# Kernel tuning notes

Measured on AMD Instinct MI355X. Metric: run time of the kernel, lower is better.

The kernel has to match this reference:

```python
import jax, jax.numpy as jnp
import numpy as np

EPS = 1e-6
LN_EPS = 1e-5


def setup_inputs() -> dict:
    key = jax.random.key(0)
    k1, k2, k3 = jax.random.split(key, 3)
    N, L, H, D = 4, 16384, 8, 16
    return {
        "queries": jax.random.normal(k1, (N, L, H, D), dtype=jnp.float32),
        "keys": jax.random.normal(k2, (N, L, H, D), dtype=jnp.float32),
        "values": jax.random.normal(k3, (N, L, H, D), dtype=jnp.float32),
        "ln_gamma": jnp.ones((D,), dtype=jnp.float32),
        "ln_beta": jnp.zeros((D,), dtype=jnp.float32),
    }


def reference(queries, keys, values, ln_gamma, ln_beta):
    initial = values  # [N, L, H, D]
    # to [N, H, L, D] and apply sigmoid feature map
    q = jax.nn.sigmoid(jnp.transpose(queries, (0, 2, 1, 3)))
    k = jax.nn.sigmoid(jnp.transpose(keys, (0, 2, 1, 3)))
    v = jnp.transpose(values, (0, 2, 1, 3))
    L = q.shape[2]
    S = k.shape[2]
    # competition/allocation normalizers (flow attention)
    normalizer_row = 1.0 / jnp.einsum('nhld,nhd->nhl', q + EPS, k.sum(axis=2) + EPS)
    normalizer_col = 1.0 / jnp.einsum('nhsd,nhd->nhs', k + EPS, q.sum(axis=2) + EPS)
    normalizer_row_refine = jnp.einsum(
        'nhld,nhd->nhl', q + EPS, (k * normalizer_col[..., None]).sum(axis=2) + EPS)
    normalizer_col_refine = jnp.einsum(
        'nhsd,nhd->nhs', k + EPS, (q * normalizer_row[..., None]).sum(axis=2) + EPS)
    normalizer_row_refine = jax.nn.sigmoid(normalizer_row_refine * (float(L) / float(S)))
    normalizer_col_refine = jax.nn.softmax(normalizer_col_refine, axis=-1) * S
    # linear attention: K^T @ (V * col_refine), then Q @ kv
    kv = jnp.einsum('nhsd,nhse->nhde', k, v * normalizer_col_refine[..., None])  # [N,H,D,D]
    x = jnp.einsum('nhld,nhde->nhle', q, kv)
    x = x * normalizer_row[..., None] * normalizer_row_refine[..., None]
    x = jnp.transpose(x, (0, 2, 1, 3))  # [N, L, H, D]
    x = initial + x
    # LayerNorm over last dim (D=16), biased variance as in torch
    mean = jnp.mean(x, axis=-1, keepdims=True)
    var = jnp.mean(jnp.square(x - mean), axis=-1, keepdims=True)
    x = (x - mean) / jnp.sqrt(var + LN_EPS) * ln_gamma + ln_beta
    return x
```

## Files before the change

### kernel.cpp

```cpp
#include <hip/hip_runtime.h>
#include <math.h>
#include <stdint.h>

constexpr int LL = 16384;
constexpr int NROW = 65536;
constexpr int NPAIR = NROW * 8;
constexpr int PAIRS_PER_N = NPAIR / 4;
constexpr float EPS = 1e-6f;
constexpr float LN_EPS = 1e-5f;

constexpr int OFF_QSUM = 0;
constexpr int OFF_KSUM = 512;
constexpr int OFF_QN   = 1024;
constexpr int OFF_KN   = 1536;
constexpr int OFF_SSUM = 2048;
constexpr int OFF_KVU  = 2080;
constexpr int STATS_FLOATS = OFF_KVU + 4 * 2048;
constexpr int FLOAT_END = 10304;
constexpr size_t MIR_Q_BYTE = (size_t)FLOAT_END * 4;
constexpr size_t MIR_ELEMS  = (size_t)NPAIR * 16;
constexpr size_t MIR_K_BYTE = MIR_Q_BYTE + MIR_ELEMS * 2;
constexpr size_t WS_FULL    = MIR_K_BYTE + MIR_ELEMS * 2;

__device__ __forceinline__ float sigm(float x) { return __fdividef(1.f, 1.f + __expf(-x)); }
__device__ __forceinline__ unsigned short f2bf(float f) {
  uint32_t x = __float_as_uint(f);
  return (unsigned short)((x + 0x7FFFu + ((x >> 16) & 1u)) >> 16);
}
__device__ __forceinline__ float bf2f(unsigned short u) {
  return __uint_as_float(((uint32_t)u) << 16);
}

template <bool MIR>
__device__ __forceinline__ void load_sig(const unsigned short* mir, const float* fp, int p, float* r) {
  if (MIR) {
    const uint4* p4 = reinterpret_cast<const uint4*>(mir + (size_t)p * 16);
    uint4 a = p4[0], b = p4[1];
    uint32_t w[8] = {a.x, a.y, a.z, a.w, b.x, b.y, b.z, b.w};
#pragma unroll
    for (int j = 0; j < 8; ++j) {
      r[2 * j]     = bf2f((unsigned short)(w[j] & 0xFFFFu));
      r[2 * j + 1] = bf2f((unsigned short)(w[j] >> 16));
    }
  } else {
    const float4* p4 = reinterpret_cast<const float4*>(fp + (size_t)p * 16);
#pragma unroll
    for (int j = 0; j < 4; ++j) {
      float4 a = p4[j];
      r[4 * j] = sigm(a.x); r[4 * j + 1] = sigm(a.y);
      r[4 * j + 2] = sigm(a.z); r[4 * j + 3] = sigm(a.w);
    }
  }
}
__device__ __forceinline__ void load_raw16(const float* fp, int p, float* r) {
  const float4* p4 = reinterpret_cast<const float4*>(fp + (size_t)p * 16);
#pragma unroll
  for (int j = 0; j < 4; ++j) {
    float4 a = p4[j];
    r[4 * j] = a.x; r[4 * j + 1] = a.y; r[4 * j + 2] = a.z; r[4 * j + 3] = a.w;
  }
}

__device__ __forceinline__ float hred(float v) {
  v += __shfl_xor(v, 8, 64);
  v += __shfl_xor(v, 16, 64);
  v += __shfl_xor(v, 32, 64);
  return v;
}

__device__ __forceinline__ void stat_atomic2(float* q, float* k, float* dQ, float* dK, int tid) {
  __shared__ float w4[4][256];
  const int wave = tid >> 6, lane = tid & 63;
#pragma unroll
  for (int d = 0; d < 16; ++d) { q[d] = hred(q[d]); k[d] = hred(k[d]); }
  if (lane < 8) {
#pragma unroll
    for (int d = 0; d < 16; ++d) {
      w4[wave][lane * 16 + d] = q[d];
      w4[wave][128 + lane * 16 + d] = k[d];
    }
  }
  __syncthreads();
  const float v = w4[0][tid] + w4[1][tid] + w4[2][tid] + w4[3][tid];
  if (tid < 128) atomicAdd(dQ + tid, v);
  else atomicAdd(dK + (tid - 128), v);
}

__device__ __forceinline__ void stat_atomic1(float* q, float* dQ, int tid) {
  __shared__ float w1[4][128];
  const int wave = tid >> 6, lane = tid & 63;
#pragma unroll
  for (int d = 0; d < 16; ++d) q[d] = hred(q[d]);
  if (lane < 8) {
#pragma unroll
    for (int d = 0; d < 16; ++d) w1[wave][lane * 16 + d] = q[d];
  }
  __syncthreads();
  if (tid < 128) atomicAdd(dQ + tid, w1[0][tid] + w1[1][tid] + w1[2][tid] + w1[3][tid]);
}

__global__ __launch_bounds__(256) void k_zero(float4* ws4) {
  const int i = blockIdx.x * 256 + threadIdx.x;
  if (i < STATS_FLOATS / 4) ws4[i] = make_float4(0.f, 0.f, 0.f, 0.f);
}

template <bool MIR>
__global__ __launch_bounds__(256) void k_prep(const float* __restrict__ Q, const float* __restrict__ K,
                                              float* __restrict__ ws,
                                              unsigned short* __restrict__ sQ, unsigned short* __restrict__ sK) {
  const int tid = threadIdx.x;
  const int n = blockIdx.x >> 7;
  const int b = blockIdx.x & 127;
  float sq[16], sk[16];
#pragma unroll
  for (int d = 0; d < 16; ++d) { sq[d] = 0.f; sk[d] = 0.f; }
#pragma unroll
  for (int c = 0; c < 4; ++c) {
    const int p = n * PAIRS_PER_N + (b * 4 + c) * 256 + tid;
    float q[16], k[16];
    load_sig<false>(nullptr, Q, p, q);
    load_sig<false>(nullptr, K, p, k);
    if (MIR) {
      union U { unsigned short u[8]; uint4 v; };
      U a, bb;
#pragma unroll
      for (int j = 0; j < 8; ++j) { a.u[j] = f2bf(q[j]); bb.u[j] = f2bf(q[8 + j]); }
      uint4* dq = reinterpret_cast<uint4*>(sQ + (size_t)p * 16);
      dq[0] = a.v; dq[1] = bb.v;
#pragma unroll
      for (int j = 0; j < 8; ++j) { a.u[j] = f2bf(k[j]); bb.u[j] = f2bf(k[8 + j]); }
      uint4* dk = reinterpret_cast<uint4*>(sK + (size_t)p * 16);
      dk[0] = a.v; dk[1] = bb.v;
    }
#pragma unroll
    for (int d = 0; d < 16; ++d) { sq[d] += q[d]; sk[d] += k[d]; }
  }
  stat_atomic2(sq, sk, ws + OFF_QSUM + n * 128, ws + OFF_KSUM + n * 128, tid);
}

template <bool MIR>
__global__ __launch_bounds__(256) void k_refq(const float* __restrict__ Q,
                                              const unsigned short* __restrict__ sQ,
                                              float* __restrict__ ws) {
  const int tid = threadIdx.x;
  const int n = blockIdx.x >> 7;
  const int b = blockIdx.x & 127;
  __shared__ float ksE[128];
  if (tid < 128) ksE[tid] = ws[OFF_KSUM + n * 128 + tid] + EPS;
  __syncthreads();
  const int h = tid & 7;
  float qn[16];
#pragma unroll
  for (int d = 0; d < 16; ++d) qn[d] = 0.f;
#pragma unroll
  for (int c = 0; c < 4; ++c) {
    const int p = n * PAIRS_PER_N + (b * 4 + c) * 256 + tid;
    float q[16];
    load_sig<MIR>(sQ, Q, p, q);
    float dr = 0.f;
#pragma unroll
    for (int d = 0; d < 16; ++d) dr += (q[d] + EPS) * ksE[h * 16 + d];
    const float nr = __fdividef(1.f, dr);
#pragma unroll
    for (int d = 0; d < 16; ++d) qn[d] += q[d] * nr;
  }
  stat_atomic1(qn, ws + OFF_QN + n * 128, tid);
}

template <bool MIR>
__global__ __launch_bounds__(256) void k_kv(const float* __restrict__ K, const float* __restrict__ V,
                                            const unsigned short* __restrict__ sK,
                                            float* __restrict__ ws) {
  const int tid = threadIdx.x;
  const int n = blockIdx.x >> 6;
  const int b = blockIdx.x & 63;
  constexpr int RS = 132;
  __shared__ float qnE[128], qsE[128];
  __shared__ float ssb[8];
  __shared__ __align__(16) float kwL[32 * RS];
  __shared__ __align__(16) float vL[32 * RS];
  if (tid < 128) {
    qnE[tid] = ws[OFF_QN + n * 128 + tid] + EPS;
    qsE[tid] = ws[OFF_QSUM + n * 128 + tid] + EPS;
  }
  if (tid < 8) ssb[tid] = 0.f;
  __syncthreads();
  const int h = tid & 7, ri = tid >> 3, lane = tid & 63;
  const int h2 = tid >> 5;
  const int d0 = ((tid >> 2) & 7) * 2;
  const int e0 = (tid & 3) * 4;
  const int base = n * PAIRS_PER_N + b * 2048;
  float acc[2][4] = {{0.f, 0.f, 0.f, 0.f}, {0.f, 0.f, 0.f, 0.f}};
  float kn[16];
#pragma unroll
  for (int d = 0; d < 16; ++d) kn[d] = 0.f;
  float kb[2][16], vb[2][16];
  load_sig<MIR>(sK, K, base + tid, kb[0]);
  load_raw16(V, base + tid, vb[0]);
#pragma unroll 2
  for (int t = 0; t < 8; ++t) {
    const int cur = t & 1, nxt = cur ^ 1;
    float* k = kb[cur];
    float* v = vb[cur];
    float dc = 0.f, ncr = 0.f;
#pragma unroll
    for (int d = 0; d < 16; ++d) {
      const float ke = k[d] + EPS;
      dc += ke * qsE[h * 16 + d];
      ncr += ke * qnE[h * 16 + d];
    }
    const float nc = __fdividef(1.f, dc);
#pragma unroll
    for (int d = 0; d < 16; ++d) kn[d] += k[d] * nc;
    const float w = __expf(ncr);
    float sw = hred(w);
    if (lane < 8) atomicAdd(&ssb[lane], sw);
    const int wb = ri * RS + h * 16;
#pragma unroll
    for (int d = 0; d < 16; ++d) { kwL[wb + d] = k[d] * w; vL[wb + d] = v[d]; }
    if (t < 7) {
      load_sig<MIR>(sK, K, base + (t + 1) * 256 + tid, kb[nxt]);
      load_raw16(V, base + (t + 1) * 256 + tid, vb[nxt]);
    }
    __syncthreads();
    const int rb0 = h2 * 16;
#pragma unroll 4
    for (int r = 0; r < 32; ++r) {
      const int rb = r * RS + rb0;
      const float2 kk = *reinterpret_cast<const float2*>(&kwL[rb + d0]);
      const float4 vv = *reinterpret_cast<const float4*>(&vL[rb + e0]);
      acc[0][0] += kk.x * vv.x; acc[0][1] += kk.x * vv.y;
      acc[0][2] += kk.x * vv.z; acc[0][3] += kk.x * vv.w;
      acc[1][0] += kk.y * vv.x; acc[1][1] += kk.y * vv.y;
      acc[1][2] += kk.y * vv.z; acc[1][3] += kk.y * vv.w;
    }
    __syncthreads();
  }
  stat_atomic1(kn, ws + OFF_KN + n * 128, tid);
  if (tid < 8) atomicAdd(&ws[OFF_SSUM + n * 8 + tid], ssb[tid]);
  float* kv = ws + OFF_KVU + n * 2048 + h2 * 256;
#pragma unroll
  for (int j = 0; j < 4; ++j) atomicAdd(&kv[d0 * 16 + e0 + j], acc[0][j]);
#pragma unroll
  for (int j = 0; j < 4; ++j) atomicAdd(&kv[(d0 + 1) * 16 + e0 + j], acc[1][j]);
}

template <bool MIR>
__global__ __launch_bounds__(256) void k_out(const float* __restrict__ Q, const float* __restrict__ V,
                                             const unsigned short* __restrict__ sQ,
                                             const float* __restrict__ gamma, const float* __restrict__ beta,
                                             const float* __restrict__ ws, float* __restrict__ out) {
  const int tid = threadIdx.x;
  const int p = blockIdx.x * 256 + tid;
  const int n = blockIdx.x >> 9;
  __shared__ __align__(16) float kvs[8 * 260];
  __shared__ float ksE[128], knE[128], gm[16], bt[16], ssE[8];
  if (tid < 8) ssE[tid] = __fdividef((float)LL, ws[OFF_SSUM + n * 8 + tid]);
  if (tid >= 8 && tid < 136) {
    const int i = tid - 8;
    ksE[i] = ws[OFF_KSUM + n * 128 + i] + EPS;
    knE[i] = ws[OFF_KN + n * 128 + i] + EPS;
  }
  if (tid >= 136 && tid < 152) gm[tid - 136] = gamma[tid - 136];
  else if (tid >= 152 && tid < 168) bt[tid - 152] = beta[tid - 152];
  __syncthreads();
  for (int i = tid; i < 2048; i += 256) {
    const int hh = i >> 8, de = i & 255;
    kvs[hh * 260 + de] = ws[OFF_KVU + n * 2048 + i] * ssE[hh];
  }
  __syncthreads();
  const int h = tid & 7;
  float q[16], v[16];
  load_sig<MIR>(sQ, Q, p, q);
  load_raw16(V, p, v);
  float dr = 0.f, drr = 0.f;
#pragma unroll
  for (int d = 0; d < 16; ++d) {
    const float qe = q[d] + EPS;
    dr += qe * ksE[h * 16 + d];
    drr += qe * knE[h * 16 + d];
  }
  const float sc = __fdividef(1.f, dr) * sigm(drr);
  float x[16];
#pragma unroll
  for (int e = 0; e < 16; ++e) x[e] = 0.f;
#pragma unroll
  for (int d = 0; d < 16; ++d) {
    const float qd = q[d];
    const float4* kr = reinterpret_cast<const float4*>(&kvs[h * 260 + d * 16]);
#pragma unroll
    for (int j = 0; j < 4; ++j) {
      float4 a = kr[j];
      x[4 * j] += qd * a.x; x[4 * j + 1] += qd * a.y;
      x[4 * j + 2] += qd * a.z; x[4 * j + 3] += qd * a.w;
    }
  }
#pragma unroll
  for (int e = 0; e < 16; ++e) x[e] = x[e] * sc + v[e];
  float mean = 0.f;
#pragma unroll
  for (int e = 0; e < 16; ++e) mean += x[e];
  mean *= (1.f / 16.f);
  float var = 0.f;
#pragma unroll
  for (int e = 0; e < 16; ++e) { const float t = x[e] - mean; var += t * t; }
  var *= (1.f / 16.f);
  const float inv = rsqrtf(var + LN_EPS);
#pragma unroll
  for (int e = 0; e < 16; ++e) x[e] = (x[e] - mean) * inv * gm[e] + bt[e];
  float4* op = reinterpret_cast<float4*>(out + (size_t)p * 16);
  op[0] = make_float4(x[0], x[1], x[2], x[3]);
  op[1] = make_float4(x[4], x[5], x[6], x[7]);
  op[2] = make_float4(x[8], x[9], x[10], x[11]);
  op[3] = make_float4(x[12], x[13], x[14], x[15]);
}

extern "C" void kernel_launch(void* const* d_in, const int* in_sizes, int n_in,
                              void* d_out, int out_size, void* d_ws, size_t ws_size,
                              hipStream_t stream) {
  const float* Q = (const float*)d_in[0];
  const float* K = (const float*)d_in[1];
  const float* V = (const float*)d_in[2];
  const float* gamma = (const float*)d_in[3];
  const float* beta = (const float*)d_in[4];
  float* ws = (float*)d_ws;
  float* out = (float*)d_out;
  unsigned short* sQ = (unsigned short*)((char*)d_ws + MIR_Q_BYTE);
  unsigned short* sK = (unsigned short*)((char*)d_ws + MIR_K_BYTE);

  const dim3 blk(256);
  const int gPrep = 512;
  const int gKv = 256;
  const int gOut = NPAIR / 256;
  const int gZero = (STATS_FLOATS / 4 + 255) / 256;

  k_zero<<<gZero, blk, 0, stream>>>(reinterpret_cast<float4*>(ws));
  if (ws_size >= WS_FULL) {
    k_prep<true><<<gPrep, blk, 0, stream>>>(Q, K, ws, sQ, sK);
    k_refq<true><<<gPrep, blk, 0, stream>>>(Q, sQ, ws);
    k_kv<true><<<gKv, blk, 0, stream>>>(K, V, sK, ws);
    k_out<true><<<gOut, blk, 0, stream>>>(Q, V, sQ, gamma, beta, ws, out);
  } else {
    k_prep<false><<<gPrep, blk, 0, stream>>>(Q, K, ws, nullptr, nullptr);
    k_refq<false><<<gPrep, blk, 0, stream>>>(Q, nullptr, ws);
    k_kv<false><<<gKv, blk, 0, stream>>>(K, V, nullptr, ws);
    k_out<false><<<gOut, blk, 0, stream>>>(Q, V, nullptr, gamma, beta, ws, out);
  }
}
```

Measured before the change: 190.8 us.

## Replicate atomic accumulators across eight slots and double k_kv grid

Global statistic accumulators (qsum, ksum, qn, kn, softmax sums, kv) are split into eight replicas indexed by block, so fewer blocks contend on the same atomic addresses. Consumer kernels sum the replicas when loading. Separately, k_kv now launches twice as many blocks, each handling half the rows, for more parallelism. The cost is extra reads of the replicas in every consumer block, a larger zeroing pass, and more atomics issued overall by k_kv.

```diff
diff --git a/kernel.cpp b/kernel.cpp
--- a/kernel.cpp
+++ b/kernel.cpp
@@ -8,15 +8,16 @@
 constexpr int PAIRS_PER_N = NPAIR / 4;
 constexpr float EPS = 1e-6f;
 constexpr float LN_EPS = 1e-5f;
+constexpr int NREP = 8;
 
 constexpr int OFF_QSUM = 0;
-constexpr int OFF_KSUM = 512;
-constexpr int OFF_QN   = 1024;
-constexpr int OFF_KN   = 1536;
-constexpr int OFF_SSUM = 2048;
-constexpr int OFF_KVU  = 2080;
-constexpr int STATS_FLOATS = OFF_KVU + 4 * 2048;
-constexpr int FLOAT_END = 10304;
+constexpr int OFF_KSUM = OFF_QSUM + 4096;
+constexpr int OFF_QN   = OFF_KSUM + 4096;
+constexpr int OFF_KN   = OFF_QN + 4096;
+constexpr int OFF_SSUM = OFF_KN + 4096;
+constexpr int OFF_KVU  = OFF_SSUM + 256;
+constexpr int STATS_FLOATS = OFF_KVU + 4 * NREP * 2048;
+constexpr int FLOAT_END = STATS_FLOATS;
 constexpr size_t MIR_Q_BYTE = (size_t)FLOAT_END * 4;
 constexpr size_t MIR_ELEMS  = (size_t)NPAIR * 16;
 constexpr size_t MIR_K_BYTE = MIR_Q_BYTE + MIR_ELEMS * 2;
@@ -97,6 +98,13 @@
   }
   __syncthreads();
   if (tid < 128) atomicAdd(dQ + tid, w1[0][tid] + w1[1][tid] + w1[2][tid] + w1[3][tid]);
+}
+
+__device__ __forceinline__ float rep_sum128(const float* base, int n, int i) {
+  float v = 0.f;
+#pragma unroll
+  for (int r = 0; r < NREP; ++r) v += base[(n * NREP + r) * 128 + i];
+  return v;
 }
 
 __global__ __launch_bounds__(256) void k_zero(float4* ws4) {
@@ -111,6 +119,7 @@
   const int tid = threadIdx.x;
   const int n = blockIdx.x >> 7;
   const int b = blockIdx.x & 127;
+  const int rep = b & (NREP - 1);
   float sq[16], sk[16];
 #pragma unroll
   for (int d = 0; d < 16; ++d) { sq[d] = 0.f; sk[d] = 0.f; }
@@ -135,7 +144,8 @@
 #pragma unroll
     for (int d = 0; d < 16; ++d) { sq[d] += q[d]; sk[d] += k[d]; }
   }
-  stat_atomic2(sq, sk, ws + OFF_QSUM + n * 128, ws + OFF_KSUM + n * 128, tid);
+  stat_atomic2(sq, sk, ws + OFF_QSUM + (n * NREP + rep) * 128,
+               ws + OFF_KSUM + (n * NREP + rep) * 128, tid);
 }
 
 template <bool MIR>
@@ -145,8 +155,9 @@
   const int tid = threadIdx.x;
   const int n = blockIdx.x >> 7;
   const int b = blockIdx.x & 127;
+  const int rep = b & (NREP - 1);
   __shared__ float ksE[128];
-  if (tid < 128) ksE[tid] = ws[OFF_KSUM + n * 128 + tid] + EPS;
+  if (tid < 128) ksE[tid] = rep_sum128(ws + OFF_KSUM, n, tid) + EPS;
   __syncthreads();
   const int h = tid & 7;
   float qn[16];
@@ -164,7 +175,7 @@
 #pragma unroll
     for (int d = 0; d < 16; ++d) qn[d] += q[d] * nr;
   }
-  stat_atomic1(qn, ws + OFF_QN + n * 128, tid);
+  stat_atomic1(qn, ws + OFF_QN + (n * NREP + rep) * 128, tid);
 }
 
 template <bool MIR>
@@ -172,16 +183,17 @@
                                             const unsigned short* __restrict__ sK,
                                             float* __restrict__ ws) {
   const int tid = threadIdx.x;
-  const int n = blockIdx.x >> 6;
-  const int b = blockIdx.x & 63;
+  const int n = blockIdx.x >> 7;
+  const int b = blockIdx.x & 127;
+  const int rep = b & (NREP - 1);
   constexpr int RS = 132;
   __shared__ float qnE[128], qsE[128];
   __shared__ float ssb[8];
   __shared__ __align__(16) float kwL[32 * RS];
   __shared__ __align__(16) float vL[32 * RS];
   if (tid < 128) {
-    qnE[tid] = ws[OFF_QN + n * 128 + tid] + EPS;
-    qsE[tid] = ws[OFF_QSUM + n * 128 + tid] + EPS;
+    qnE[tid] = rep_sum128(ws + OFF_QN, n, tid) + EPS;
+    qsE[tid] = rep_sum128(ws + OFF_QSUM, n, tid) + EPS;
   }
   if (tid < 8) ssb[tid] = 0.f;
   __syncthreads();
@@ -189,7 +201,7 @@
   const int h2 = tid >> 5;
   const int d0 = ((tid >> 2) & 7) * 2;
   const int e0 = (tid & 3) * 4;
-  const int base = n * PAIRS_PER_N + b * 2048;
+  const int base = n * PAIRS_PER_N + b * 1024;
   float acc[2][4] = {{0.f, 0.f, 0.f, 0.f}, {0.f, 0.f, 0.f, 0.f}};
   float kn[16];
 #pragma unroll
@@ -198,7 +210,7 @@
   load_sig<MIR>(sK, K, base + tid, kb[0]);
   load_raw16(V, base + tid, vb[0]);
 #pragma unroll 2
-  for (int t = 0; t < 8; ++t) {
+  for (int t = 0; t < 4; ++t) {
     const int cur = t & 1, nxt = cur ^ 1;
     float* k = kb[cur];
     float* v = vb[cur];
@@ -218,7 +230,7 @@
     const int wb = ri * RS + h * 16;
 #pragma unroll
     for (int d = 0; d < 16; ++d) { kwL[wb + d] = k[d] * w; vL[wb + d] = v[d]; }
-    if (t < 7) {
+    if (t < 3) {
       load_sig<MIR>(sK, K, base + (t + 1) * 256 + tid, kb[nxt]);
       load_raw16(V, base + (t + 1) * 256 + tid, vb[nxt]);
     }
@@ -236,9 +248,9 @@
     }
     __syncthreads();
   }
-  stat_atomic1(kn, ws + OFF_KN + n * 128, tid);
-  if (tid < 8) atomicAdd(&ws[OFF_SSUM + n * 8 + tid], ssb[tid]);
-  float* kv = ws + OFF_KVU + n * 2048 + h2 * 256;
+  stat_atomic1(kn, ws + OFF_KN + (n * NREP + rep) * 128, tid);
+  if (tid < 8) atomicAdd(&ws[OFF_SSUM + (n * NREP + rep) * 8 + tid], ssb[tid]);
+  float* kv = ws + OFF_KVU + (size_t)(n * NREP + rep) * 2048 + h2 * 256;
 #pragma unroll
   for (int j = 0; j < 4; ++j) atomicAdd(&kv[d0 * 16 + e0 + j], acc[0][j]);
 #pragma unroll
@@ -255,18 +267,26 @@
   const int n = blockIdx.x >> 9;
   __shared__ __align__(16) float kvs[8 * 260];
   __shared__ float ksE[128], knE[128], gm[16], bt[16], ssE[8];
-  if (tid < 8) ssE[tid] = __fdividef((float)LL, ws[OFF_SSUM + n * 8 + tid]);
+  if (tid < 8) {
+    float ss = 0.f;
+#pragma unroll
+    for (int r = 0; r < NREP; ++r) ss += ws[OFF_SSUM + (n * NREP + r) * 8 + tid];
+    ssE[tid] = __fdividef((float)LL, ss);
+  }
   if (tid >= 8 && tid < 136) {
     const int i = tid - 8;
-    ksE[i] = ws[OFF_KSUM + n * 128 + i] + EPS;
-    knE[i] = ws[OFF_KN + n * 128 + i] + EPS;
+    ksE[i] = rep_sum128(ws + OFF_KSUM, n, i) + EPS;
+    knE[i] = rep_sum128(ws + OFF_KN, n, i) + EPS;
   }
   if (tid >= 136 && tid < 152) gm[tid - 136] = gamma[tid - 136];
   else if (tid >= 152 && tid < 168) bt[tid - 152] = beta[tid - 152];
   __syncthreads();
   for (int i = tid; i < 2048; i += 256) {
     const int hh = i >> 8, de = i & 255;
-    kvs[hh * 260 + de] = ws[OFF_KVU + n * 2048 + i] * ssE[hh];
+    float acc = 0.f;
+#pragma unroll
+    for (int r = 0; r < NREP; ++r) acc += ws[OFF_KVU + (size_t)(n * NREP + r) * 2048 + i];
+    kvs[hh * 260 + de] = acc * ssE[hh];
   }
   __syncthreads();
   const int h = tid & 7;
@@ -330,7 +350,7 @@
 
   const dim3 blk(256);
   const int gPrep = 512;
-  const int gKv = 256;
+  const int gKv = 512;
   const int gOut = NPAIR / 256;
   const int gZero = (STATS_FLOATS / 4 + 255) / 256;
 
```

After: 202.4 us. 1.06x slower.

## Replace global atomics with per-block partials and add a reduction kernel

Applied to the files above, without the earlier changes.

Each stats kernel now writes per-block partial sums to workspace instead of atomically adding into shared totals. Consumers reduce those partials on load, and a new k_kvred kernel folds the kv, kn, softmax-sum and ksum partials. This removes the zeroing kernel and the atomic contention. It also lets k_kv run with four times as many blocks, each handling 512 pairs, for better occupancy. In exchange the workspace grows, there is one extra launch, and every block of k_refq and k_kv redundantly re-reduces the partials.

```diff
diff --git a/kernel.cpp b/kernel.cpp
--- a/kernel.cpp
+++ b/kernel.cpp
@@ -9,14 +9,16 @@
 constexpr float EPS = 1e-6f;
 constexpr float LN_EPS = 1e-5f;
 
-constexpr int OFF_QSUM = 0;
-constexpr int OFF_KSUM = 512;
-constexpr int OFF_QN   = 1024;
-constexpr int OFF_KN   = 1536;
-constexpr int OFF_SSUM = 2048;
-constexpr int OFF_KVU  = 2080;
-constexpr int STATS_FLOATS = OFF_KVU + 4 * 2048;
-constexpr int FLOAT_END = 10304;
+constexpr int F_KSUM = 0;
+constexpr int F_KN   = 512;
+constexpr int F_SS   = 1024;
+constexpr int F_KV   = 1056;
+constexpr int P_A1 = 9472;
+constexpr int P_A2 = P_A1 + 4 * 128 * 256;
+constexpr int P_KN = P_A2 + 4 * 128 * 128;
+constexpr int P_SS = P_KN + 4 * 256 * 128;
+constexpr int P_KV = P_SS + 4 * 256 * 8;
+constexpr int FLOAT_END = P_KV + 4 * 256 * 2048;
 constexpr size_t MIR_Q_BYTE = (size_t)FLOAT_END * 4;
 constexpr size_t MIR_ELEMS  = (size_t)NPAIR * 16;
 constexpr size_t MIR_K_BYTE = MIR_Q_BYTE + MIR_ELEMS * 2;
@@ -68,40 +70,33 @@
   return v;
 }
 
-__device__ __forceinline__ void stat_atomic2(float* q, float* k, float* dQ, float* dK, int tid) {
-  __shared__ float w4[4][256];
+__device__ __forceinline__ void stat_partial2(float* a, float* b, float* w4 ,
+                                              float* dst, int tid) {
   const int wave = tid >> 6, lane = tid & 63;
 #pragma unroll
-  for (int d = 0; d < 16; ++d) { q[d] = hred(q[d]); k[d] = hred(k[d]); }
+  for (int d = 0; d < 16; ++d) { a[d] = hred(a[d]); b[d] = hred(b[d]); }
   if (lane < 8) {
 #pragma unroll
     for (int d = 0; d < 16; ++d) {
-      w4[wave][lane * 16 + d] = q[d];
-      w4[wave][128 + lane * 16 + d] = k[d];
+      w4[wave * 256 + lane * 16 + d] = a[d];
+      w4[wave * 256 + 128 + lane * 16 + d] = b[d];
     }
   }
   __syncthreads();
-  const float v = w4[0][tid] + w4[1][tid] + w4[2][tid] + w4[3][tid];
-  if (tid < 128) atomicAdd(dQ + tid, v);
-  else atomicAdd(dK + (tid - 128), v);
-}
-
-__device__ __forceinline__ void stat_atomic1(float* q, float* dQ, int tid) {
-  __shared__ float w1[4][128];
+  dst[tid] = w4[tid] + w4[256 + tid] + w4[512 + tid] + w4[768 + tid];
+}
+
+__device__ __forceinline__ void stat_partial1(float* a, float* w1 ,
+                                              float* dst, int tid) {
   const int wave = tid >> 6, lane = tid & 63;
 #pragma unroll
-  for (int d = 0; d < 16; ++d) q[d] = hred(q[d]);
+  for (int d = 0; d < 16; ++d) a[d] = hred(a[d]);
   if (lane < 8) {
 #pragma unroll
-    for (int d = 0; d < 16; ++d) w1[wave][lane * 16 + d] = q[d];
+    for (int d = 0; d < 16; ++d) w1[wave * 128 + lane * 16 + d] = a[d];
   }
   __syncthreads();
-  if (tid < 128) atomicAdd(dQ + tid, w1[0][tid] + w1[1][tid] + w1[2][tid] + w1[3][tid]);
-}
-
-__global__ __launch_bounds__(256) void k_zero(float4* ws4) {
-  const int i = blockIdx.x * 256 + threadIdx.x;
-  if (i < STATS_FLOATS / 4) ws4[i] = make_float4(0.f, 0.f, 0.f, 0.f);
+  if (tid < 128) dst[tid] = w1[tid] + w1[128 + tid] + w1[256 + tid] + w1[384 + tid];
 }
 
 template <bool MIR>
@@ -111,6 +106,7 @@
   const int tid = threadIdx.x;
   const int n = blockIdx.x >> 7;
   const int b = blockIdx.x & 127;
+  __shared__ float w4[1024];
   float sq[16], sk[16];
 #pragma unroll
   for (int d = 0; d < 16; ++d) { sq[d] = 0.f; sk[d] = 0.f; }
@@ -135,7 +131,7 @@
 #pragma unroll
     for (int d = 0; d < 16; ++d) { sq[d] += q[d]; sk[d] += k[d]; }
   }
-  stat_atomic2(sq, sk, ws + OFF_QSUM + n * 128, ws + OFF_KSUM + n * 128, tid);
+  stat_partial2(sq, sk, w4, ws + P_A1 + (size_t)blockIdx.x * 256, tid);
 }
 
 template <bool MIR>
@@ -146,8 +142,18 @@
   const int n = blockIdx.x >> 7;
   const int b = blockIdx.x & 127;
   __shared__ float ksE[128];
-  if (tid < 128) ksE[tid] = ws[OFF_KSUM + n * 128 + tid] + EPS;
-  __syncthreads();
+  __shared__ float w1[512];
+  {
+    const int i = tid & 127, half = tid >> 7;
+    float a = 0.f;
+    const float* src = ws + P_A1 + ((size_t)(n * 128 + half * 64)) * 256 + 128 + i;
+#pragma unroll 4
+    for (int c = 0; c < 64; ++c) a += src[(size_t)c * 256];
+    w1[tid] = a;
+    __syncthreads();
+    if (tid < 128) ksE[tid] = w1[tid] + w1[128 + tid] + EPS;
+    __syncthreads();
+  }
   const int h = tid & 7;
   float qn[16];
 #pragma unroll
@@ -164,7 +170,7 @@
 #pragma unroll
     for (int d = 0; d < 16; ++d) qn[d] += q[d] * nr;
   }
-  stat_atomic1(qn, ws + OFF_QN + n * 128, tid);
+  stat_partial1(qn, w1, ws + P_A2 + (size_t)blockIdx.x * 128, tid);
 }
 
 template <bool MIR>
@@ -172,24 +178,39 @@
                                             const unsigned short* __restrict__ sK,
                                             float* __restrict__ ws) {
   const int tid = threadIdx.x;
-  const int n = blockIdx.x >> 6;
-  const int b = blockIdx.x & 63;
+  const int n = blockIdx.x >> 8;
+  const int b = blockIdx.x & 255;
   constexpr int RS = 132;
   __shared__ float qnE[128], qsE[128];
   __shared__ float ssb[8];
+  __shared__ float w1[512];
   __shared__ __align__(16) float kwL[32 * RS];
   __shared__ __align__(16) float vL[32 * RS];
-  if (tid < 128) {
-    qnE[tid] = ws[OFF_QN + n * 128 + tid] + EPS;
-    qsE[tid] = ws[OFF_QSUM + n * 128 + tid] + EPS;
-  }
-  if (tid < 8) ssb[tid] = 0.f;
-  __syncthreads();
+  {
+    const int i = tid & 127, half = tid >> 7;
+    float a = 0.f;
+    const float* src = ws + P_A1 + ((size_t)(n * 128 + half * 64)) * 256 + i;
+#pragma unroll 4
+    for (int c = 0; c < 64; ++c) a += src[(size_t)c * 256];
+    w1[tid] = a;
+    __syncthreads();
+    if (tid < 128) qsE[tid] = w1[tid] + w1[128 + tid] + EPS;
+    __syncthreads();
+    float bb = 0.f;
+    const float* src2 = ws + P_A2 + ((size_t)(n * 128 + half * 64)) * 128 + i;
+#pragma unroll 4
+    for (int c = 0; c < 64; ++c) bb += src2[(size_t)c * 128];
+    w1[tid] = bb;
+    __syncthreads();
+    if (tid < 128) qnE[tid] = w1[tid] + w1[128 + tid] + EPS;
+    if (tid < 8) ssb[tid] = 0.f;
+    __syncthreads();
+  }
   const int h = tid & 7, ri = tid >> 3, lane = tid & 63;
   const int h2 = tid >> 5;
   const int d0 = ((tid >> 2) & 7) * 2;
   const int e0 = (tid & 3) * 4;
-  const int base = n * PAIRS_PER_N + b * 2048;
+  const int base = n * PAIRS_PER_N + b * 512;
   float acc[2][4] = {{0.f, 0.f, 0.f, 0.f}, {0.f, 0.f, 0.f, 0.f}};
   float kn[16];
 #pragma unroll
@@ -197,11 +218,10 @@
   float kb[2][16], vb[2][16];
   load_sig<MIR>(sK, K, base + tid, kb[0]);
   load_raw16(V, base + tid, vb[0]);
-#pragma unroll 2
-  for (int t = 0; t < 8; ++t) {
-    const int cur = t & 1, nxt = cur ^ 1;
-    float* k = kb[cur];
-    float* v = vb[cur];
+#pragma unroll
+  for (int t = 0; t < 2; ++t) {
+    float* k = kb[t];
+    float* v = vb[t];
     float dc = 0.f, ncr = 0.f;
 #pragma unroll
     for (int d = 0; d < 16; ++d) {
@@ -218,9 +238,9 @@
     const int wb = ri * RS + h * 16;
 #pragma unroll
     for (int d = 0; d < 16; ++d) { kwL[wb + d] = k[d] * w; vL[wb + d] = v[d]; }
-    if (t < 7) {
-      load_sig<MIR>(sK, K, base + (t + 1) * 256 + tid, kb[nxt]);
-      load_raw16(V, base + (t + 1) * 256 + tid, vb[nxt]);
+    if (t < 1) {
+      load_sig<MIR>(sK, K, base + 256 + tid, kb[1]);
+      load_raw16(V, base + 256 + tid, vb[1]);
     }
     __syncthreads();
     const int rb0 = h2 * 16;
@@ -236,13 +256,46 @@
     }
     __syncthreads();
   }
-  stat_atomic1(kn, ws + OFF_KN + n * 128, tid);
-  if (tid < 8) atomicAdd(&ws[OFF_SSUM + n * 8 + tid], ssb[tid]);
-  float* kv = ws + OFF_KVU + n * 2048 + h2 * 256;
-#pragma unroll
-  for (int j = 0; j < 4; ++j) atomicAdd(&kv[d0 * 16 + e0 + j], acc[0][j]);
-#pragma unroll
-  for (int j = 0; j < 4; ++j) atomicAdd(&kv[(d0 + 1) * 16 + e0 + j], acc[1][j]);
+  stat_partial1(kn, w1, ws + P_KN + (size_t)blockIdx.x * 128, tid);
+  if (tid < 8) ws[P_SS + (size_t)blockIdx.x * 8 + tid] = ssb[tid];
+  float* pk = ws + P_KV + (size_t)blockIdx.x * 2048;
+  *reinterpret_cast<float4*>(pk + h2 * 256 + d0 * 16 + e0) =
+      make_float4(acc[0][0], acc[0][1], acc[0][2], acc[0][3]);
+  *reinterpret_cast<float4*>(pk + h2 * 256 + (d0 + 1) * 16 + e0) =
+      make_float4(acc[1][0], acc[1][1], acc[1][2], acc[1][3]);
+}
+
+__global__ __launch_bounds__(256) void k_kvred(float* __restrict__ ws) {
+  const int tid = threadIdx.x;
+  const int n = blockIdx.x >> 3, seg = blockIdx.x & 7;
+  {
+    float a = 0.f;
+    const float* src = ws + P_KV + (size_t)n * 256 * 2048 + seg * 256 + tid;
+#pragma unroll 4
+    for (int c = 0; c < 256; ++c) a += src[(size_t)c * 2048];
+    ws[F_KV + n * 2048 + seg * 256 + tid] = a;
+  }
+  if (seg == 0 && tid < 128) {
+    float s = 0.f;
+    const float* src = ws + P_KN + (size_t)n * 256 * 128 + tid;
+#pragma unroll 4
+    for (int c = 0; c < 256; ++c) s += src[(size_t)c * 128];
+    ws[F_KN + n * 128 + tid] = s;
+  }
+  if (seg == 1 && tid < 8) {
+    float s = 0.f;
+    const float* src = ws + P_SS + (size_t)n * 256 * 8 + tid;
+#pragma unroll 4
+    for (int c = 0; c < 256; ++c) s += src[(size_t)c * 8];
+    ws[F_SS + n * 8 + tid] = s;
+  }
+  if (seg == 2 && tid < 128) {
+    float s = 0.f;
+    const float* src = ws + P_A1 + (size_t)n * 128 * 256 + 128 + tid;
+#pragma unroll 4
+    for (int c = 0; c < 128; ++c) s += src[(size_t)c * 256];
+    ws[F_KSUM + n * 128 + tid] = s;
+  }
 }
 
 template <bool MIR>
@@ -255,18 +308,18 @@
   const int n = blockIdx.x >> 9;
   __shared__ __align__(16) float kvs[8 * 260];
   __shared__ float ksE[128], knE[128], gm[16], bt[16], ssE[8];
-  if (tid < 8) ssE[tid] = __fdividef((float)LL, ws[OFF_SSUM + n * 8 + tid]);
+  if (tid < 8) ssE[tid] = __fdividef((float)LL, ws[F_SS + n * 8 + tid]);
   if (tid >= 8 && tid < 136) {
     const int i = tid - 8;
-    ksE[i] = ws[OFF_KSUM + n * 128 + i] + EPS;
-    knE[i] = ws[OFF_KN + n * 128 + i] + EPS;
+    ksE[i] = ws[F_KSUM + n * 128 + i] + EPS;
+    knE[i] = ws[F_KN + n * 128 + i] + EPS;
   }
   if (tid >= 136 && tid < 152) gm[tid - 136] = gamma[tid - 136];
   else if (tid >= 152 && tid < 168) bt[tid - 152] = beta[tid - 152];
   __syncthreads();
   for (int i = tid; i < 2048; i += 256) {
     const int hh = i >> 8, de = i & 255;
-    kvs[hh * 260 + de] = ws[OFF_KVU + n * 2048 + i] * ssE[hh];
+    kvs[hh * 260 + de] = ws[F_KV + n * 2048 + i] * ssE[hh];
   }
   __syncthreads();
   const int h = tid & 7;
@@ -330,20 +383,20 @@
 
   const dim3 blk(256);
   const int gPrep = 512;
-  const int gKv = 256;
+  const int gKv = 1024;
   const int gOut = NPAIR / 256;
-  const int gZero = (STATS_FLOATS / 4 + 255) / 256;
-
-  k_zero<<<gZero, blk, 0, stream>>>(reinterpret_cast<float4*>(ws));
+
   if (ws_size >= WS_FULL) {
     k_prep<true><<<gPrep, blk, 0, stream>>>(Q, K, ws, sQ, sK);
     k_refq<true><<<gPrep, blk, 0, stream>>>(Q, sQ, ws);
     k_kv<true><<<gKv, blk, 0, stream>>>(K, V, sK, ws);
+    k_kvred<<<32, blk, 0, stream>>>(ws);
     k_out<true><<<gOut, blk, 0, stream>>>(Q, V, sQ, gamma, beta, ws, out);
   } else {
     k_prep<false><<<gPrep, blk, 0, stream>>>(Q, K, ws, nullptr, nullptr);
     k_refq<false><<<gPrep, blk, 0, stream>>>(Q, nullptr, ws);
     k_kv<false><<<gKv, blk, 0, stream>>>(K, V, nullptr, ws);
+    k_kvred<<<32, blk, 0, stream>>>(ws);
     k_out<false><<<gOut, blk, 0, stream>>>(Q, V, nullptr, gamma, beta, ws, out);
   }
 }
```

New measurement: 234.8 us. +23.1%, slower.

## Replace float atomics with per-block partials and last-block reductions

Applied to the files above, without the earlier changes.

Each stats kernel now writes per-block partial sums to workspace slots. A counter-based last-block pattern lets the final block of each batch reduce those partials and write the totals, replacing float atomicAdd accumulation. This also removes the separate zeroing kernel launch. The counters are never reset, so correctness relies on the modulo-TARGET wraparound and on the workspace starting at zero. The final reduction now runs serially in a single block per batch.

```diff
diff --git a/kernel.cpp b/kernel.cpp
--- a/kernel.cpp
+++ b/kernel.cpp
@@ -8,17 +8,24 @@
 constexpr int PAIRS_PER_N = NPAIR / 4;
 constexpr float EPS = 1e-6f;
 constexpr float LN_EPS = 1e-5f;
-
-constexpr int OFF_QSUM = 0;
-constexpr int OFF_KSUM = 512;
-constexpr int OFF_QN   = 1024;
-constexpr int OFF_KN   = 1536;
-constexpr int OFF_SSUM = 2048;
-constexpr int OFF_KVU  = 2080;
-constexpr int STATS_FLOATS = OFF_KVU + 4 * 2048;
-constexpr int FLOAT_END = 10304;
+constexpr size_t MIR_ELEMS = (size_t)NPAIR * 16;
+
+constexpr int F_KSUM = 0;
+constexpr int F_KN   = 512;
+constexpr int F_SS   = 1024;
+constexpr int F_QSUM = 1056;
+constexpr int F_QN   = 1568;
+constexpr int F_KV   = 2080;
+constexpr int CNT_A  = 10272;
+constexpr int CNT_B  = 10276;
+constexpr int CNT_C  = 10280;
+constexpr int P_A1 = 10304;
+constexpr int P_A2 = P_A1 + 512 * 256;
+constexpr int P_KN = P_A2 + 512 * 128;
+constexpr int P_SS = P_KN + 256 * 128;
+constexpr int P_KV = P_SS + 256 * 8;
+constexpr int FLOAT_END = P_KV + 256 * 2048;
 constexpr size_t MIR_Q_BYTE = (size_t)FLOAT_END * 4;
-constexpr size_t MIR_ELEMS  = (size_t)NPAIR * 16;
 constexpr size_t MIR_K_BYTE = MIR_Q_BYTE + MIR_ELEMS * 2;
 constexpr size_t WS_FULL    = MIR_K_BYTE + MIR_ELEMS * 2;
 
@@ -60,6 +67,14 @@
     r[4 * j] = a.x; r[4 * j + 1] = a.y; r[4 * j + 2] = a.z; r[4 * j + 3] = a.w;
   }
 }
+__device__ __forceinline__ void pack_store(unsigned short* dst, int p, const float* r) {
+  union U { unsigned short u[8]; uint4 v; };
+  U a, b;
+#pragma unroll
+  for (int j = 0; j < 8; ++j) { a.u[j] = f2bf(r[j]); b.u[j] = f2bf(r[8 + j]); }
+  uint4* d = reinterpret_cast<uint4*>(dst + (size_t)p * 16);
+  d[0] = a.v; d[1] = b.v;
+}
 
 __device__ __forceinline__ float hred(float v) {
   v += __shfl_xor(v, 8, 64);
@@ -68,40 +83,47 @@
   return v;
 }
 
-__device__ __forceinline__ void stat_atomic2(float* q, float* k, float* dQ, float* dK, int tid) {
-  __shared__ float w4[4][256];
+__device__ __forceinline__ void stat_partial2(float* a, float* b, float* w4 ,
+                                              float* dst, int tid) {
   const int wave = tid >> 6, lane = tid & 63;
 #pragma unroll
-  for (int d = 0; d < 16; ++d) { q[d] = hred(q[d]); k[d] = hred(k[d]); }
+  for (int d = 0; d < 16; ++d) { a[d] = hred(a[d]); b[d] = hred(b[d]); }
   if (lane < 8) {
 #pragma unroll
     for (int d = 0; d < 16; ++d) {
-      w4[wave][lane * 16 + d] = q[d];
-      w4[wave][128 + lane * 16 + d] = k[d];
-    }
-  }
-  __syncthreads();
-  const float v = w4[0][tid] + w4[1][tid] + w4[2][tid] + w4[3][tid];
-  if (tid < 128) atomicAdd(dQ + tid, v);
-  else atomicAdd(dK + (tid - 128), v);
-}
-
-__device__ __forceinline__ void stat_atomic1(float* q, float* dQ, int tid) {
-  __shared__ float w1[4][128];
+      w4[wave * 256 + lane * 16 + d] = a[d];
+      w4[wave * 256 + 128 + lane * 16 + d] = b[d];
+    }
+  }
+  __syncthreads();
+  dst[tid] = w4[tid] + w4[256 + tid] + w4[512 + tid] + w4[768 + tid];
+}
+
+__device__ __forceinline__ void stat_partial1(float* a, float* w1 ,
+                                              float* dst, int tid) {
   const int wave = tid >> 6, lane = tid & 63;
 #pragma unroll
-  for (int d = 0; d < 16; ++d) q[d] = hred(q[d]);
+  for (int d = 0; d < 16; ++d) a[d] = hred(a[d]);
   if (lane < 8) {
 #pragma unroll
-    for (int d = 0; d < 16; ++d) w1[wave][lane * 16 + d] = q[d];
-  }
-  __syncthreads();
-  if (tid < 128) atomicAdd(dQ + tid, w1[0][tid] + w1[1][tid] + w1[2][tid] + w1[3][tid]);
-}
-
-__global__ __launch_bounds__(256) void k_zero(float4* ws4) {
-  const int i = blockIdx.x * 256 + threadIdx.x;
-  if (i < STATS_FLOATS / 4) ws4[i] = make_float4(0.f, 0.f, 0.f, 0.f);
+    for (int d = 0; d < 16; ++d) w1[wave * 128 + lane * 16 + d] = a[d];
+  }
+  __syncthreads();
+  if (tid < 128) dst[tid] = w1[tid] + w1[128 + tid] + w1[256 + tid] + w1[384 + tid];
+}
+
+template <unsigned int TARGET>
+__device__ __forceinline__ bool last_block(unsigned int* cnt, int tid, unsigned int* flag) {
+  __threadfence();
+  __syncthreads();
+  if (tid == 0) {
+    const unsigned int old = atomicAdd(cnt, 1u);
+    *flag = (((old + 1u) & (TARGET - 1u)) == 0u) ? 1u : 0u;
+  }
+  __syncthreads();
+  const bool last = (*flag != 0u);
+  if (last) __threadfence();
+  return last;
 }
 
 template <bool MIR>
@@ -111,6 +133,8 @@
   const int tid = threadIdx.x;
   const int n = blockIdx.x >> 7;
   const int b = blockIdx.x & 127;
+  __shared__ float w4[1024];
+  __shared__ unsigned int flag;
   float sq[16], sk[16];
 #pragma unroll
   for (int d = 0; d < 16; ++d) { sq[d] = 0.f; sk[d] = 0.f; }
@@ -120,22 +144,20 @@
     float q[16], k[16];
     load_sig<false>(nullptr, Q, p, q);
     load_sig<false>(nullptr, K, p, k);
-    if (MIR) {
-      union U { unsigned short u[8]; uint4 v; };
-      U a, bb;
-#pragma unroll
-      for (int j = 0; j < 8; ++j) { a.u[j] = f2bf(q[j]); bb.u[j] = f2bf(q[8 + j]); }
-      uint4* dq = reinterpret_cast<uint4*>(sQ + (size_t)p * 16);
-      dq[0] = a.v; dq[1] = bb.v;
-#pragma unroll
-      for (int j = 0; j < 8; ++j) { a.u[j] = f2bf(k[j]); bb.u[j] = f2bf(k[8 + j]); }
-      uint4* dk = reinterpret_cast<uint4*>(sK + (size_t)p * 16);
-      dk[0] = a.v; dk[1] = bb.v;
-    }
+    if (MIR) { pack_store(sQ, p, q); pack_store(sK, p, k); }
 #pragma unroll
     for (int d = 0; d < 16; ++d) { sq[d] += q[d]; sk[d] += k[d]; }
   }
-  stat_atomic2(sq, sk, ws + OFF_QSUM + n * 128, ws + OFF_KSUM + n * 128, tid);
+  stat_partial2(sq, sk, w4, ws + P_A1 + (size_t)blockIdx.x * 256, tid);
+  unsigned int* cnt = reinterpret_cast<unsigned int*>(ws) + CNT_A + n;
+  if (last_block<128u>(cnt, tid, &flag)) {
+    float acc = 0.f;
+    const float* src = ws + P_A1 + (size_t)n * 128 * 256 + tid;
+#pragma unroll 8
+    for (int c = 0; c < 128; ++c) acc += src[(size_t)c * 256];
+    if (tid < 128) ws[F_QSUM + n * 128 + tid] = acc;
+    else ws[F_KSUM + n * 128 + (tid - 128)] = acc;
+  }
 }
 
 template <bool MIR>
@@ -146,7 +168,9 @@
   const int n = blockIdx.x >> 7;
   const int b = blockIdx.x & 127;
   __shared__ float ksE[128];
-  if (tid < 128) ksE[tid] = ws[OFF_KSUM + n * 128 + tid] + EPS;
+  __shared__ float w1[512];
+  __shared__ unsigned int flag;
+  if (tid < 128) ksE[tid] = ws[F_KSUM + n * 128 + tid] + EPS;
   __syncthreads();
   const int h = tid & 7;
   float qn[16];
@@ -164,7 +188,18 @@
 #pragma unroll
     for (int d = 0; d < 16; ++d) qn[d] += q[d] * nr;
   }
-  stat_atomic1(qn, ws + OFF_QN + n * 128, tid);
+  stat_partial1(qn, w1, ws + P_A2 + (size_t)blockIdx.x * 128, tid);
+  unsigned int* cnt = reinterpret_cast<unsigned int*>(ws) + CNT_B + n;
+  if (last_block<128u>(cnt, tid, &flag)) {
+    const int col = tid & 127, half = tid >> 7;
+    float acc = 0.f;
+    const float* src = ws + P_A2 + (size_t)(n * 128 + half * 64) * 128 + col;
+#pragma unroll 8
+    for (int c = 0; c < 64; ++c) acc += src[(size_t)c * 128];
+    if (half) w1[col] = acc;
+    __syncthreads();
+    if (!half) ws[F_QN + n * 128 + col] = acc + w1[col];
+  }
 }
 
 template <bool MIR>
@@ -177,11 +212,13 @@
   constexpr int RS = 132;
   __shared__ float qnE[128], qsE[128];
   __shared__ float ssb[8];
+  __shared__ float w1[512];
   __shared__ __align__(16) float kwL[32 * RS];
   __shared__ __align__(16) float vL[32 * RS];
+  __shared__ unsigned int flag;
   if (tid < 128) {
-    qnE[tid] = ws[OFF_QN + n * 128 + tid] + EPS;
-    qsE[tid] = ws[OFF_QSUM + n * 128 + tid] + EPS;
+    qnE[tid] = ws[F_QN + n * 128 + tid] + EPS;
+    qsE[tid] = ws[F_QSUM + n * 128 + tid] + EPS;
   }
   if (tid < 8) ssb[tid] = 0.f;
   __syncthreads();
@@ -236,13 +273,42 @@
     }
     __syncthreads();
   }
-  stat_atomic1(kn, ws + OFF_KN + n * 128, tid);
-  if (tid < 8) atomicAdd(&ws[OFF_SSUM + n * 8 + tid], ssb[tid]);
-  float* kv = ws + OFF_KVU + n * 2048 + h2 * 256;
-#pragma unroll
-  for (int j = 0; j < 4; ++j) atomicAdd(&kv[d0 * 16 + e0 + j], acc[0][j]);
-#pragma unroll
-  for (int j = 0; j < 4; ++j) atomicAdd(&kv[(d0 + 1) * 16 + e0 + j], acc[1][j]);
+  stat_partial1(kn, w1, ws + P_KN + (size_t)blockIdx.x * 128, tid);
+  if (tid < 8) ws[P_SS + (size_t)blockIdx.x * 8 + tid] = ssb[tid];
+  float* pk = ws + P_KV + (size_t)blockIdx.x * 2048;
+  *reinterpret_cast<float4*>(pk + h2 * 256 + d0 * 16 + e0) =
+      make_float4(acc[0][0], acc[0][1], acc[0][2], acc[0][3]);
+  *reinterpret_cast<float4*>(pk + h2 * 256 + (d0 + 1) * 16 + e0) =
+      make_float4(acc[1][0], acc[1][1], acc[1][2], acc[1][3]);
+  unsigned int* cnt = reinterpret_cast<unsigned int*>(ws) + CNT_C + n;
+  if (last_block<64u>(cnt, tid, &flag)) {
+    float a8[8];
+#pragma unroll
+    for (int j = 0; j < 8; ++j) a8[j] = 0.f;
+    const float* srcKV = ws + P_KV + (size_t)n * 64 * 2048;
+#pragma unroll 2
+    for (int c = 0; c < 64; ++c) {
+      const float* s = srcKV + (size_t)c * 2048 + tid;
+#pragma unroll
+      for (int j = 0; j < 8; ++j) a8[j] += s[j * 256];
+    }
+#pragma unroll
+    for (int j = 0; j < 8; ++j) ws[F_KV + n * 2048 + j * 256 + tid] = a8[j];
+    if (tid < 128) {
+      float a = 0.f;
+      const float* s = ws + P_KN + (size_t)n * 64 * 128 + tid;
+#pragma unroll 8
+      for (int c = 0; c < 64; ++c) a += s[(size_t)c * 128];
+      ws[F_KN + n * 128 + tid] = a;
+    }
+    if (tid < 8) {
+      float a = 0.f;
+      const float* s = ws + P_SS + (size_t)n * 64 * 8 + tid;
+#pragma unroll 8
+      for (int c = 0; c < 64; ++c) a += s[(size_t)c * 8];
+      ws[F_SS + n * 8 + tid] = a;
+    }
+  }
 }
 
 template <bool MIR>
@@ -255,18 +321,18 @@
   const int n = blockIdx.x >> 9;
   __shared__ __align__(16) float kvs[8 * 260];
   __shared__ float ksE[128], knE[128], gm[16], bt[16], ssE[8];
-  if (tid < 8) ssE[tid] = __fdividef((float)LL, ws[OFF_SSUM + n * 8 + tid]);
+  if (tid < 8) ssE[tid] = __fdividef((float)LL, ws[F_SS + n * 8 + tid]);
   if (tid >= 8 && tid < 136) {
     const int i = tid - 8;
-    ksE[i] = ws[OFF_KSUM + n * 128 + i] + EPS;
-    knE[i] = ws[OFF_KN + n * 128 + i] + EPS;
+    ksE[i] = ws[F_KSUM + n * 128 + i] + EPS;
+    knE[i] = ws[F_KN + n * 128 + i] + EPS;
   }
   if (tid >= 136 && tid < 152) gm[tid - 136] = gamma[tid - 136];
   else if (tid >= 152 && tid < 168) bt[tid - 152] = beta[tid - 152];
   __syncthreads();
   for (int i = tid; i < 2048; i += 256) {
     const int hh = i >> 8, de = i & 255;
-    kvs[hh * 260 + de] = ws[OFF_KVU + n * 2048 + i] * ssE[hh];
+    kvs[hh * 260 + de] = ws[F_KV + n * 2048 + i] * ssE[hh];
   }
   __syncthreads();
   const int h = tid & 7;
@@ -332,9 +398,7 @@
   const int gPrep = 512;
   const int gKv = 256;
   const int gOut = NPAIR / 256;
-  const int gZero = (STATS_FLOATS / 4 + 255) / 256;
-
-  k_zero<<<gZero, blk, 0, stream>>>(reinterpret_cast<float4*>(ws));
+
   if (ws_size >= WS_FULL) {
     k_prep<true><<<gPrep, blk, 0, stream>>>(Q, K, ws, sQ, sK);
     k_refq<true><<<gPrep, blk, 0, stream>>>(Q, sQ, ws);
```

Result: slower. 334.0 us (+75.1%).
